# Optimization experiments

Hardware: AMD Instinct MI355X
Metric: run time of the kernel (lower is better)

The kernel has to match this reference:

```python
import jax, jax.numpy as jnp
import numpy as np

N = 128000      # total nodes
B = 128         # graphs, 1000 nodes each
L = 4           # max_levels
S_MAX = 1000    # max cluster size (<= PositionalEncoding max_len)
H = 128         # hidden dim (all conv output dims equal)
IN_DIM = 128
OUT_DIM = 1
E = 1024000
TEMP = 0.1


def layer_norm(x, g, b, eps=1e-5):
    mu = jnp.mean(x, axis=-1, keepdims=True)
    v = jnp.mean((x - mu) ** 2, axis=-1, keepdims=True)
    return (x - mu) * jax.lax.rsqrt(v + eps) * g + b


def transformer_conv(x, src, dst, Wq, bq, Wk, bk, Wv, bv, Ws, bs):
    # PyG TransformerConv, heads=1: softmax over in-edges of each dst node
    q = x @ Wq + bq
    k = x @ Wk + bk
    v = x @ Wv + bv
    logits = jnp.sum(q[dst] * k[src], axis=-1) / jnp.sqrt(jnp.float32(q.shape[-1]))
    m = jax.ops.segment_max(logits, dst, num_segments=N)
    e = jnp.exp(logits - m[dst])
    s = jax.ops.segment_sum(e, dst, num_segments=N)
    alpha = e / s[dst]
    agg = jax.ops.segment_sum(alpha[:, None] * v[src], dst, num_segments=N)
    return agg + x @ Ws + bs  # root_weight skip connection


def pos_encoding(S, d):
    pos = jnp.arange(S, dtype=jnp.float32)[:, None]
    div = jnp.exp(jnp.arange(0, d, 2, dtype=jnp.float32) * (-jnp.log(10000.0) / d))
    pe = jnp.zeros((S, d), jnp.float32)
    pe = pe.at[:, 0::2].set(jnp.sin(pos * div))
    pe = pe.at[:, 1::2].set(jnp.cos(pos * div))
    return pe


def gru(xseq, Wih, Whh, bih, bhh):
    # xseq: [G, S, H] -> outputs [G, S, H]; torch GRU gate math
    G = xseq.shape[0]
    def step(h, x_t):
        gi = x_t @ Wih.T + bih
        gh = h @ Whh.T + bhh
        ir, iz, inn = jnp.split(gi, 3, axis=-1)
        hr, hz, hn = jnp.split(gh, 3, axis=-1)
        r = jax.nn.sigmoid(ir + hr)
        z = jax.nn.sigmoid(iz + hz)
        n = jnp.tanh(inn + r * hn)
        h_new = (1.0 - z) * n + z * h
        return h_new, h_new
    h0 = jnp.zeros((G, Whh.shape[1]), xseq.dtype)
    _, outs = jax.lax.scan(step, h0, jnp.swapaxes(xseq, 0, 1))
    return jnp.swapaxes(outs, 0, 1)


def _forward(x, tree_edge_index, call_sequences, batch,
             conv_Wq, conv_bq, conv_Wk, conv_bk, conv_Wv, conv_bv, conv_Ws, conv_bs,
             ln_g, ln_b, centers, proj_W, proj_b,
             gru_Wih, gru_Whh, gru_bih, gru_bhh, seqln_g, seqln_b,
             lin1_W, lin1_b, lin2_W, lin2_b):
    src, dst = tree_edge_index[0], tree_edge_index[1]
    h = x
    for i in range(3):  # conv1/bn1, conv2/bn2, conv4/bn4
        h = transformer_conv(h, src, dst, conv_Wq[i], conv_bq[i], conv_Wk[i],
                             conv_bk[i], conv_Wv[i], conv_bv[i], conv_Ws[i], conv_bs[i])
        h = jax.nn.relu(layer_norm(h, ln_g[i], ln_b[i]))

    # HierarchicalClassifier: cosine-sim soft assignment + center variance loss
    xn = h / jnp.maximum(jnp.linalg.norm(h, axis=-1, keepdims=True), 1e-8)
    cn = centers / jnp.maximum(jnp.linalg.norm(centers, axis=-1, keepdims=True), 1e-8)
    assign = jax.nn.softmax((xn @ cn.T) / TEMP, axis=-1)
    level_ids = jnp.argmax(assign, axis=1).astype(jnp.int32)
    iu0, iu1 = np.triu_indices(L, k=1)
    dvec = jnp.linalg.norm(centers[iu0] - centers[iu1], axis=-1)
    distance = -jnp.var(dvec, ddof=1)  # torch.var is unbiased

    # ragged gather + pad: group nodes by (graph, cluster), sort by call order
    G = B * L
    group = batch * L + level_ids                       # [N]
    order = jnp.argsort(group * N + call_sequences)     # sort by group, then call
    g_sorted = group[order]
    counts = jax.ops.segment_sum(jnp.ones((N,), jnp.int32), group, num_segments=G)
    starts = jnp.cumsum(counts) - counts
    pos = jnp.arange(N, dtype=jnp.int32) - starts[g_sorted]
    seq = jnp.zeros((G, S_MAX, H), h.dtype).at[g_sorted, pos].set(h[order])

    # SequentialRNN: proj -> pos-enc -> GRU -> LayerNorm -> ReLU (mask unused)
    sin = seq @ proj_W + proj_b + pos_encoding(S_MAX, H)[None]
    outs = gru(sin, gru_Wih, gru_Whh, gru_bih, gru_bhh)
    outs = jax.nn.relu(layer_norm(outs, seqln_g, seqln_b))

    # scatter valid positions back; singleton clusters keep raw features
    node_out = jnp.zeros_like(h).at[order].set(outs[g_sorted, pos])
    singleton = (counts[group] == 1)
    gout = jnp.where(singleton[:, None], h, node_out)

    y = jax.nn.gelu(gout @ lin1_W + lin1_b, approximate=False)
    y = jax.nn.sigmoid(y @ lin2_W + lin2_b)
    return y, distance


def setup_inputs():
    key = jax.random.key(0)
    ks = jax.random.split(key, 16)
    p = lambda k, s: jax.random.normal(k, s, jnp.float32) * 0.02
    return {
        "x": jax.random.normal(ks[0], (N, IN_DIM), jnp.float32),
        "tree_edge_index": jax.random.randint(ks[1], (2, E), 0, N, dtype=jnp.int32),
        "call_sequences": jax.random.permutation(ks[2], N).astype(jnp.int32),
        "batch": (jnp.arange(N, dtype=jnp.int32) * B) // N,  # 1000 nodes per graph
        "conv_Wq": p(ks[3], (3, H, H)), "conv_bq": jnp.zeros((3, H), jnp.float32),
        "conv_Wk": p(ks[4], (3, H, H)), "conv_bk": jnp.zeros((3, H), jnp.float32),
        "conv_Wv": p(ks[5], (3, H, H)), "conv_bv": jnp.zeros((3, H), jnp.float32),
        "conv_Ws": p(ks[6], (3, H, H)), "conv_bs": jnp.zeros((3, H), jnp.float32),
        "ln_g": jnp.ones((3, H), jnp.float32), "ln_b": jnp.zeros((3, H), jnp.float32),
        "centers": jax.random.normal(ks[7], (L, H), jnp.float32),
        "proj_W": p(ks[8], (H, H)), "proj_b": jnp.zeros((H,), jnp.float32),
        "gru_Wih": p(ks[9], (3 * H, H)), "gru_Whh": p(ks[10], (3 * H, H)),
        "gru_bih": jnp.zeros((3 * H,), jnp.float32), "gru_bhh": jnp.zeros((3 * H,), jnp.float32),
        "seqln_g": jnp.ones((H,), jnp.float32), "seqln_b": jnp.zeros((H,), jnp.float32),
        "lin1_W": p(ks[11], (H, 8)), "lin1_b": jnp.zeros((8,), jnp.float32),
        "lin2_W": p(ks[12], (8, OUT_DIM)), "lin2_b": jnp.zeros((OUT_DIM,), jnp.float32),
    }


def reference(x, tree_edge_index, call_sequences, batch,
              conv_Wq, conv_bq, conv_Wk, conv_bk, conv_Wv, conv_bv, conv_Ws, conv_bs,
              ln_g, ln_b, centers, proj_W, proj_b,
              gru_Wih, gru_Whh, gru_bih, gru_bhh, seqln_g, seqln_b,
              lin1_W, lin1_b, lin2_W, lin2_b):
    return _forward(x, tree_edge_index, call_sequences, batch,
                    conv_Wq, conv_bq, conv_Wk, conv_bk, conv_Wv, conv_bv, conv_Ws, conv_bs,
                    ln_g, ln_b, centers, proj_W, proj_b,
                    gru_Wih, gru_Whh, gru_bih, gru_bhh, seqln_g, seqln_b,
                    lin1_W, lin1_b, lin2_W, lin2_b)
```

## Files before the change

### kernel.cpp

```cpp
#include <hip/hip_runtime.h>

#define NN 128000
#define EE 1024000
#define HH 128
#define GG 512
#define SMAX 1000
#define NCHUNK 500

typedef unsigned int u32;
typedef unsigned short u16;

constexpr size_t NH     = (size_t)NN*HH;
constexpr size_t F_H    = 0;
constexpr size_t F_A    = NH;
constexpr size_t F_B    = 2*NH;
constexpr size_t F_NODE = F_A + (size_t)NN*192;
constexpr size_t F_CN   = 3*NH;
constexpr size_t F_WKT  = F_CN   + 512;
constexpr size_t F_WQK  = F_WKT  + 3*16384;
constexpr size_t F_BQK  = F_WQK  + 3*16384;
constexpr size_t F_CW   = F_BQK  + 3*128;
constexpr size_t F_PEW  = F_CW   + 128*384;
constexpr size_t F_PEB  = F_PEW  + 1000*384;
constexpr size_t F_END  = F_PEB  + 1000*128;

constexpr size_t I_ROWP = 0;
constexpr size_t I_CUR  = I_ROWP + NN + 8;
constexpr size_t I_COL  = I_CUR  + NN;
constexpr size_t I_GRP  = I_COL  + EE;
constexpr size_t I_INV  = I_GRP  + NN;
constexpr size_t I_POS  = I_INV  + NN;
constexpr size_t I_GN   = I_POS  + NN;
constexpr size_t I_CNT  = I_GN   + (size_t)GG*SMAX;
constexpr size_t I_CH   = I_CNT  + GG;
constexpr size_t I_BS   = I_CH   + (size_t)NCHUNK*GG;
constexpr size_t I_WT   = I_BS   + 512;
constexpr size_t I_END  = I_WT   + 64*384;

constexpr size_t WS_NEEDED = F_END*4 + I_END*4;

__device__ inline float wredf(float v){
  #pragma unroll
  for (int o = 32; o; o >>= 1) v += __shfl_xor(v, o);
  return v;
}
__device__ inline u32 bf16rne(float f){
  u32 u = __float_as_uint(f);
  return (u + 0x7fffu + ((u >> 16) & 1u)) >> 16;
}
__device__ inline float bf2f(u16 u){
  return __uint_as_float(((u32)u) << 16);
}
__device__ inline float frcp(float x){
#if __has_builtin(__builtin_amdgcn_rcpf)
  return __builtin_amdgcn_rcpf(x);
#else
  return 1.f / x;
#endif
}

typedef _Float16 h2_t __attribute__((ext_vector_type(2)));
__device__ inline float dot2f(u32 w, u32 h, float acc){
#if __has_builtin(__builtin_amdgcn_fdot2)
  return __builtin_amdgcn_fdot2(__builtin_bit_cast(h2_t, w),
                                __builtin_bit_cast(h2_t, h), acc, false);
#else
  float r;
  asm("v_dot2_f32_f16 %0, %1, %2, %3" : "=v"(r) : "v"(w), "v"(h), "v"(acc));
  return r;
#endif
}
#define PIN4(v) asm volatile("" : "+v"((v).x), "+v"((v).y), "+v"((v).z), "+v"((v).w))

__global__ void k_sentinel(float* __restrict__ out, int n, float val){
  int i = blockIdx.x * 256 + threadIdx.x;
  if (i < n) out[i] = val;
}

__global__ void k_zero(int* __restrict__ p){
  p[blockIdx.x * 256 + threadIdx.x] = 0;
}
__global__ void k_hist(const int* __restrict__ dst, int* __restrict__ deg){
  int e = blockIdx.x * 256 + threadIdx.x;
  atomicAdd(&deg[dst[e]], 1);
}
__global__ void k_s1(const int* __restrict__ deg, int* __restrict__ bsum){
  __shared__ int red[256];
  int t = threadIdx.x;
  red[t] = deg[blockIdx.x * 256 + t];
  __syncthreads();
  for (int s = 128; s; s >>= 1){ if (t < s) red[t] += red[t + s]; __syncthreads(); }
  if (!t) bsum[blockIdx.x] = red[0];
}
__global__ void k_s2(int* __restrict__ bsum){
  __shared__ int arr[512];
  int t = threadIdx.x;
  int v0 = (t < NCHUNK) ? bsum[t] : 0;
  arr[t] = v0; __syncthreads();
  for (int off = 1; off < 512; off <<= 1){
    int v = (t >= off) ? arr[t - off] : 0;
    __syncthreads();
    arr[t] += v;
    __syncthreads();
  }
  if (t < NCHUNK) bsum[t] = arr[t] - v0;
}
__global__ void k_s3(const int* __restrict__ bsum, int* __restrict__ row_ptr,
                     int* __restrict__ cursor){
  __shared__ int arr[256];
  int t = threadIdx.x;
  int i = blockIdx.x * 256 + t;
  int v0 = cursor[i];
  arr[t] = v0; __syncthreads();
  for (int off = 1; off < 256; off <<= 1){
    int v = (t >= off) ? arr[t - off] : 0;
    __syncthreads();
    arr[t] += v;
    __syncthreads();
  }
  int exc = arr[t] - v0 + bsum[blockIdx.x];
  row_ptr[i] = exc;
  cursor[i]  = exc;
  if (i == 0) row_ptr[NN] = EE;
}
__global__ void k_scatter(const int* __restrict__ src, const int* __restrict__ dst,
                          int* __restrict__ cursor, int* __restrict__ col){
  int e = blockIdx.x * 256 + threadIdx.x;
  int idx = atomicAdd(&cursor[dst[e]], 1);
  col[idx] = src[e];
}

__global__ void k_setup(const float* __restrict__ centers, float* __restrict__ cn,
                        float* __restrict__ dist_out){
  __shared__ float red[128];
  int t = threadIdx.x;
  for (int l = 0; l < 4; ++l){
    float v = centers[l*128 + t];
    red[t] = v * v; __syncthreads();
    for (int s = 64; s; s >>= 1){ if (t < s) red[t] += red[t + s]; __syncthreads(); }
    float nrm = sqrtf(red[0]);
    __syncthreads();
    cn[l*128 + t] = v / fmaxf(nrm, 1e-8f);
  }
  const int iu0[6] = {0,0,0,1,1,2}, iu1[6] = {1,2,3,2,3,3};
  __shared__ float dv[6];
  for (int p = 0; p < 6; ++p){
    float d = centers[iu0[p]*128 + t] - centers[iu1[p]*128 + t];
    red[t] = d * d; __syncthreads();
    for (int s = 64; s; s >>= 1){ if (t < s) red[t] += red[t + s]; __syncthreads(); }
    if (!t) dv[p] = sqrtf(red[0]);
    __syncthreads();
  }
  if (!t){
    float mean = 0.f;
    for (int p = 0; p < 6; ++p) mean += dv[p];
    mean /= 6.f;
    float var = 0.f;
    for (int p = 0; p < 6; ++p){ float d = dv[p] - mean; var += d * d; }
    var /= 5.f;
    dist_out[0] = -var;
  }
}

__global__ void k_pe(const float* __restrict__ projb, float* __restrict__ peb){
  int p = blockIdx.x, t = threadIdx.x;
  float ex  = (float)(t >> 1) * (-2.0f * 9.210340371976184f / 128.0f);
  float ang = (float)p * expf(ex);
  float v = (t & 1) ? cosf(ang) : sinf(ang);
  peb[p*128 + t] = v + projb[t];
}
__global__ void k_pew(const float* __restrict__ peb, const float* __restrict__ Wih,
                      const float* __restrict__ bih, float* __restrict__ pew){
  int p = blockIdx.x;
  int j = blockIdx.y * 128 + threadIdx.x;
  const float* pb = peb + p*128;
  const float* wr = Wih + (size_t)j*128;
  float acc = bih[j];
  #pragma unroll 4
  for (int m = 0; m < 128; ++m) acc += pb[m] * wr[m];
  pew[(size_t)p*384 + j] = acc;
}
__global__ void k_combw(const float* __restrict__ projW, const float* __restrict__ Wih,
                        float* __restrict__ cw){
  int kk = blockIdx.x;
  int j  = blockIdx.y * 128 + threadIdx.x;
  const float* pr = projW + (size_t)kk*128;
  const float* wr = Wih + (size_t)j*128;
  float acc = 0.f;
  #pragma unroll 4
  for (int m = 0; m < 128; ++m) acc += pr[m] * wr[m];
  cw[(size_t)kk*384 + j] = acc;
}
__global__ void k_tr(const float* __restrict__ Wk, float* __restrict__ wkt){
  int kk = blockIdx.x, l = blockIdx.y, c = threadIdx.x;
  wkt[(size_t)l*16384 + kk*128 + c] = Wk[(size_t)l*16384 + c*128 + kk];
}
__global__ void k_mv(const float* __restrict__ M, const float* __restrict__ v,
                     float* __restrict__ out){
  int l = blockIdx.x, i = threadIdx.x;
  const float* row = M + (size_t)l*16384 + (size_t)i*128;
  const float* vv = v + l*128;
  float acc = 0.f;
  #pragma unroll 4
  for (int j = 0; j < 128; ++j) acc += row[j] * vv[j];
  out[l*128 + i] = acc;
}
__global__ void k_packwhh16(const float* __restrict__ Whh, u32* __restrict__ wt){
  int kp = blockIdx.x;
  int j  = blockIdx.y * 128 + threadIdx.x;
  _Float16 a = (_Float16)Whh[(size_t)j*128 + 2*kp];
  _Float16 b = (_Float16)Whh[(size_t)j*128 + 2*kp + 1];
  u32 lo = (u32)__builtin_bit_cast(u16, a);
  u32 hi = (u32)__builtin_bit_cast(u16, b);
  wt[(size_t)j*64 + kp] = (hi << 16) | lo;
}

__global__ __launch_bounds__(256, 2) void k_gemm(
    const float* __restrict__ X, const float* __restrict__ W, int ldw,
    const float* __restrict__ X2, const float* __restrict__ W2,
    const float* __restrict__ bias, const float* __restrict__ pew,
    const int* __restrict__ pos, float* __restrict__ out,
    u16* __restrict__ outb, int ldo,
    const float* __restrict__ lng, const float* __restrict__ lnb,
    const float* __restrict__ bvv, const int* __restrict__ rowp){
  __shared__ __align__(16) float Wl[64*132];
  __shared__ __align__(16) float Xl[64*132];
  int tid = threadIdx.x;
  int rb = blockIdx.x * 128;
  int cb = blockIdx.y * 128;
  int rg = tid >> 4;
  int cg = tid & 15;
  int kxor = (cg >> 2) & 3;
  float acc[8][8];
  #pragma unroll
  for (int a = 0; a < 8; ++a)
    #pragma unroll
    for (int b = 0; b < 8; ++b) acc[a][b] = 0.f;
  int nhalf = X2 ? 4 : 2;
  for (int half = 0; half < nhalf; ++half){
    const float* Xs = (half < 2) ? X : X2;
    const float* Ws = (half < 2) ? W : W2;
    int ldws = (half < 2) ? ldw : 128;
    int hk = half & 1;
    __syncthreads();
    #pragma unroll
    for (int it = 0; it < 8; ++it){
      int idx = it*256 + tid;
      int kk = idx >> 5, c4 = idx & 31;
      *(float4*)&Wl[kk*132 + c4*4] =
          *(const float4*)&Ws[(size_t)(hk*64 + kk)*ldws + cb + c4*4];
    }
    #pragma unroll
    for (int it = 0; it < 8; ++it){
      int idx = it*256 + tid;
      int r = idx >> 4, c4 = idx & 15;
      float4 xv = *(const float4*)&Xs[(size_t)(rb + r)*128 + hk*64 + c4*4];
      Xl[(c4*4+0)*132 + r] = xv.x;
      Xl[(c4*4+1)*132 + r] = xv.y;
      Xl[(c4*4+2)*132 + r] = xv.z;
      Xl[(c4*4+3)*132 + r] = xv.w;
    }
    __syncthreads();
    #pragma unroll 2
    for (int kk = 0; kk < 64; ++kk){
      int kx = kk ^ kxor;
      float4 wa = *(const float4*)&Wl[kx*132 + cg*8];
      float4 wb = *(const float4*)&Wl[kx*132 + cg*8 + 4];
      float4 xa = *(const float4*)&Xl[kx*132 + rg*8];
      float4 xb = *(const float4*)&Xl[kx*132 + rg*8 + 4];
      float xs[8] = {xa.x, xa.y, xa.z, xa.w, xb.x, xb.y, xb.z, xb.w};
      float ws[8] = {wa.x, wa.y, wa.z, wa.w, wb.x, wb.y, wb.z, wb.w};
      #pragma unroll
      for (int rr = 0; rr < 8; ++rr)
        #pragma unroll
        for (int j = 0; j < 8; ++j) acc[rr][j] += xs[rr] * ws[j];
    }
  }
  if (lng){
    float gv[8], bl[8], bb[8], vv[8];
    #pragma unroll
    for (int j = 0; j < 8; ++j){
      int c = cg*8 + j;
      gv[j] = lng[c]; bl[j] = lnb[c]; bb[j] = bias[c]; vv[j] = bvv[c];
    }
    #pragma unroll
    for (int rr = 0; rr < 8; ++rr){
      int r = rb + rg*8 + rr;
      bool deg = rowp[r+1] > rowp[r];
      float rs = 0.f, rq = 0.f;
      #pragma unroll
      for (int j = 0; j < 8; ++j){
        float v = acc[rr][j] + bb[j] + (deg ? vv[j] : 0.f);
        acc[rr][j] = v;
        rs += v; rq += v*v;
      }
      #pragma unroll
      for (int o = 8; o; o >>= 1){ rs += __shfl_xor(rs, o); rq += __shfl_xor(rq, o); }
      float mu = rs * 0.0078125f;
      float var = rq * 0.0078125f - mu*mu;
      float rstd = rsqrtf(var + 1e-5f);
      float ov[8];
      #pragma unroll
      for (int j = 0; j < 8; ++j)
        ov[j] = fmaxf((acc[rr][j] - mu)*rstd*gv[j] + bl[j], 0.f);
      float* op = out + (size_t)r*128 + cg*8;
      *(float4*)op       = *(const float4*)&ov[0];
      *(float4*)(op + 4) = *(const float4*)&ov[4];
    }
    return;
  }
  #pragma unroll
  for (int rr = 0; rr < 8; ++rr){
    int r = rb + rg*8 + rr;
    float bv[8];
    if (pos){
      const float* pw = pew + (size_t)pos[r]*384 + cb + cg*8;
      #pragma unroll
      for (int j = 0; j < 8; ++j) bv[j] = pw[j];
    } else if (bias){
      #pragma unroll
      for (int j = 0; j < 8; ++j) bv[j] = bias[cb + cg*8 + j];
    } else {
      #pragma unroll
      for (int j = 0; j < 8; ++j) bv[j] = 0.f;
    }
    if (outb){
      u16 ob[8];
      #pragma unroll
      for (int j = 0; j < 8; ++j) ob[j] = (u16)bf16rne(acc[rr][j] + bv[j]);
      *(uint4*)(outb + (size_t)r*ldo + cb + cg*8) = *(const uint4*)ob;
    } else {
      float ov[8];
      #pragma unroll
      for (int j = 0; j < 8; ++j) ov[j] = acc[rr][j] + bv[j];
      float* op = out + (size_t)r*ldo + cb + cg*8;
      *(float4*)op       = *(const float4*)&ov[0];
      *(float4*)(op + 4) = *(const float4*)&ov[4];
    }
  }
}

__global__ __launch_bounds__(256) void k_edge(
    const float* __restrict__ qt, const float* __restrict__ xsrc,
    const int* __restrict__ row_ptr, const int* __restrict__ col,
    float* __restrict__ xagg){
  int d = blockIdx.x * 8 + (threadIdx.x >> 5);
  int lane = threadIdx.x & 31;
  int e0 = row_ptr[d], e1 = row_ptr[d+1];
  if (e0 == e1){
    *(float4*)&xagg[(size_t)d*128 + lane*4] = make_float4(0.f, 0.f, 0.f, 0.f);
    return;
  }
  const float S = 0.08838834764831845f;
  float4 qv = *(const float4*)&qt[(size_t)d*128 + lane*4];
  float ss0 = 0.f, ss1 = 0.f;
  float4 A0 = make_float4(0.f,0.f,0.f,0.f), A1 = make_float4(0.f,0.f,0.f,0.f);
  int e = e0;
  for (; e + 1 < e1; e += 2){
    float4 x0 = *(const float4*)&xsrc[(size_t)col[e]  *128 + lane*4];
    float4 x1 = *(const float4*)&xsrc[(size_t)col[e+1]*128 + lane*4];
    float p0 = qv.x*x0.x + qv.y*x0.y + qv.z*x0.z + qv.w*x0.w;
    float p1 = qv.x*x1.x + qv.y*x1.y + qv.z*x1.z + qv.w*x1.w;
    #pragma unroll
    for (int o = 16; o; o >>= 1){ p0 += __shfl_xor(p0, o); p1 += __shfl_xor(p1, o); }
    float el0 = __expf(p0 * S);
    float el1 = __expf(p1 * S);
    ss0 += el0; ss1 += el1;
    A0.x += el0*x0.x; A0.y += el0*x0.y; A0.z += el0*x0.z; A0.w += el0*x0.w;
    A1.x += el1*x1.x; A1.y += el1*x1.y; A1.z += el1*x1.z; A1.w += el1*x1.w;
  }
  if (e < e1){
    float4 x0 = *(const float4*)&xsrc[(size_t)col[e]*128 + lane*4];
    float p0 = qv.x*x0.x + qv.y*x0.y + qv.z*x0.z + qv.w*x0.w;
    #pragma unroll
    for (int o = 16; o; o >>= 1) p0 += __shfl_xor(p0, o);
    float el0 = __expf(p0 * S);
    ss0 += el0;
    A0.x += el0*x0.x; A0.y += el0*x0.y; A0.z += el0*x0.z; A0.w += el0*x0.w;
  }
  float inv = 1.f / (ss0 + ss1);
  *(float4*)&xagg[(size_t)d*128 + lane*4] =
      make_float4((A0.x+A1.x)*inv, (A0.y+A1.y)*inv, (A0.z+A1.z)*inv, (A0.w+A1.w)*inv);
}

__global__ __launch_bounds__(256) void k_lnrelu_cls(
    const float* __restrict__ in, const float* __restrict__ g,
    const float* __restrict__ b, const float* __restrict__ bvv,
    const int* __restrict__ rowp, float* __restrict__ outp,
    const float* __restrict__ cn, const int* __restrict__ batch,
    const int* __restrict__ callsq, int* __restrict__ grp, int* __restrict__ inv){
  int node = blockIdx.x * 4 + (threadIdx.x >> 6);
  int lane = threadIdx.x & 63;
  float x0 = in[(size_t)node*128 + 2*lane], x1 = in[(size_t)node*128 + 2*lane + 1];
  if (rowp[node+1] > rowp[node]){
    x0 += bvv[2*lane];
    x1 += bvv[2*lane + 1];
  }
  float s = wredf(x0 + x1);
  float qq = wredf(x0*x0 + x1*x1);
  float mu = s * 0.0078125f;
  float var = qq * 0.0078125f - mu*mu;
  float rstd = rsqrtf(var + 1e-5f);
  float y0 = fmaxf((x0 - mu)*rstd*g[2*lane]   + b[2*lane],   0.f);
  float y1 = fmaxf((x1 - mu)*rstd*g[2*lane+1] + b[2*lane+1], 0.f);
  outp[(size_t)node*128 + 2*lane]     = y0;
  outp[(size_t)node*128 + 2*lane + 1] = y1;
  float p0 = y0*cn[      2*lane] + y1*cn[      2*lane+1];
  float p1 = y0*cn[128 + 2*lane] + y1*cn[128 + 2*lane+1];
  float p2 = y0*cn[256 + 2*lane] + y1*cn[256 + 2*lane+1];
  float p3 = y0*cn[384 + 2*lane] + y1*cn[384 + 2*lane+1];
  p0 = wredf(p0); p1 = wredf(p1); p2 = wredf(p2); p3 = wredf(p3);
  if (lane == 0){
    float best = p0; int bi = 0;
    if (p1 > best){ best = p1; bi = 1; }
    if (p2 > best){ best = p2; bi = 2; }
    if (p3 > best){ best = p3; bi = 3; }
    grp[node] = batch[node]*4 + bi;
    inv[callsq[node]] = node;
  }
}

__global__ __launch_bounds__(256) void k_g1(const int* __restrict__ inv,
                                            const int* __restrict__ grp,
                                            int* __restrict__ ch){
  __shared__ int hist[GG];
  int c = blockIdx.x, t = threadIdx.x;
  hist[t] = 0; hist[t + 256] = 0;
  __syncthreads();
  int g = grp[inv[c*256 + t]];
  atomicAdd(&hist[g], 1);
  __syncthreads();
  ch[c*GG + t] = hist[t];
  ch[c*GG + 256 + t] = hist[256 + t];
}
__global__ void k_g2(int* __restrict__ ch, int* __restrict__ cnt){
  __shared__ int arr[512];
  int g = blockIdx.x, t = threadIdx.x;
  int v0 = (t < NCHUNK) ? ch[(size_t)t*GG + g] : 0;
  arr[t] = v0; __syncthreads();
  for (int off = 1; off < 512; off <<= 1){
    int v = (t >= off) ? arr[t - off] : 0;
    __syncthreads();
    arr[t] += v;
    __syncthreads();
  }
  if (t < NCHUNK) ch[(size_t)t*GG + g] = arr[t] - v0;
  if (t == 511) cnt[g] = arr[511];
}
__global__ __launch_bounds__(256) void k_g3(
    const int* __restrict__ inv, const int* __restrict__ grp,
    const int* __restrict__ ch, int* __restrict__ pos, int* __restrict__ gn){
  __shared__ int hist[GG];
  int c = blockIdx.x, t = threadIdx.x;
  hist[t] = 0; hist[t + 256] = 0;
  __syncthreads();
  int node = inv[c*256 + t];
  int g = grp[node];
  int lane = t & 63, w = t >> 6;
  int before = 0, total = 0;
  for (int j = 0; j < 64; ++j){
    int gj = __shfl(g, j);
    if (gj == g){ total++; if (j < lane) before++; }
  }
  int base = 0;
  for (int wv = 0; wv < 4; ++wv){
    if (w == wv){
      base = hist[g];
      if (before == total - 1) hist[g] = base + total;
    }
    __syncthreads();
  }
  int p = ch[c*GG + g] + base + before;
  pos[node] = p;
  gn[(size_t)g*SMAX + p] = node;
}

__global__ __launch_bounds__(256)
__attribute__((amdgpu_waves_per_eu(2, 2)))
void k_gru(
    const u16* __restrict__ gi, const u32* __restrict__ wt,
    const float* __restrict__ bhh, const int* __restrict__ gn,
    const int* __restrict__ cnt, u16* __restrict__ node_out){
  __shared__ __align__(16) u16 hb16[2][128];
  int t = threadIdx.x;
  int j = t >> 1;
  int kh = t & 1;
  int g = blockIdx.x;
  int my = cnt[g];
  if (my <= 1) return;
  uint4 wr_[8], wz_[8], wn_[8];
  {
    const uint4* wt4 = (const uint4*)wt;
    size_t b0 = (size_t)(0*128 + j)*16 + kh*8;
    size_t b1 = (size_t)(1*128 + j)*16 + kh*8;
    size_t b2 = (size_t)(2*128 + j)*16 + kh*8;
    #pragma unroll
    for (int s = 0; s < 8; ++s){
      wr_[s] = wt4[b0 + s];
      wz_[s] = wt4[b1 + s];
      wn_[s] = wt4[b2 + s];
    }
    #pragma unroll
    for (int s = 0; s < 8; ++s){
      PIN4(wr_[s]); PIN4(wz_[s]); PIN4(wn_[s]);
    }
  }
  if (t < 128) hb16[0][t] = 0;
  float br = bhh[j], bz = bhh[128 + j], bn = bhh[256 + j];
  const int* gnr = gn + (size_t)g*SMAX;
  float hprev = 0.f;
  int nA = gnr[0];
  int nB = gnr[min(1, my - 1)];
  int nC = gnr[min(2, my - 1)];
  const u16* gA = gi + (size_t)nA*384;
  const u16* gB = gi + (size_t)nB*384;
  const u16* gC = gi + (size_t)nC*384;
  float axr = bf2f(gA[j]), axz = bf2f(gA[128 + j]), axn = bf2f(gA[256 + j]);
  float bxr = bf2f(gB[j]), bxz = bf2f(gB[128 + j]), bxn = bf2f(gB[256 + j]);
  float cxr = bf2f(gC[j]), cxz = bf2f(gC[128 + j]), cxn = bf2f(gC[256 + j]);
  __syncthreads();
  for (int p = 0; p < my; ++p){
    int cur = p & 1, nxt = cur ^ 1;
    float xr = axr, xz = axz, xn = axn;
    int node = nA;
    axr = bxr; axz = bxz; axn = bxn; nA = nB;
    bxr = cxr; bxz = cxz; bxn = cxn; nB = nC;
    nC = gnr[min(p + 3, my - 1)];
    const u16* gN = gi + (size_t)nC*384;
    cxr = bf2f(gN[j]); cxz = bf2f(gN[128 + j]); cxn = bf2f(gN[256 + j]);
    const uint4* HB = (const uint4*)&hb16[cur][0];
    uint4 hh[8];
    #pragma unroll
    for (int s = 0; s < 8; ++s) hh[s] = HB[kh*8 + s];
    __builtin_amdgcn_s_setprio(1);
    float ar = 0.f, az = 0.f, an = 0.f;
    #pragma unroll
    for (int s = 0; s < 8; ++s){
      ar = dot2f(wr_[s].x, hh[s].x, ar); az = dot2f(wz_[s].x, hh[s].x, az); an = dot2f(wn_[s].x, hh[s].x, an);
      ar = dot2f(wr_[s].y, hh[s].y, ar); az = dot2f(wz_[s].y, hh[s].y, az); an = dot2f(wn_[s].y, hh[s].y, an);
      ar = dot2f(wr_[s].z, hh[s].z, ar); az = dot2f(wz_[s].z, hh[s].z, az); an = dot2f(wn_[s].z, hh[s].z, an);
      ar = dot2f(wr_[s].w, hh[s].w, ar); az = dot2f(wz_[s].w, hh[s].w, az); an = dot2f(wn_[s].w, hh[s].w, an);
    }
    ar += __shfl_xor(ar, 1); az += __shfl_xor(az, 1); an += __shfl_xor(an, 1);
    ar += br; az += bz; an += bn;
    float er = __expf(-(xr + ar));
    float r  = frcp(1.f + er);
    float ez = __expf(-(xz + az));
    float z  = frcp(1.f + ez);
    float y  = xn + r * an;
    float e2 = __expf(-2.f * y);
    float n  = (1.f - e2) * frcp(1.f + e2);
    float hnew = n + z * (hprev - n);
    __builtin_amdgcn_s_setprio(0);
    hprev = hnew;
    if (!kh){
      _Float16 hf = (_Float16)hnew;
      hb16[nxt][j] = __builtin_bit_cast(u16, hf);
      node_out[(size_t)node*128 + j] = (u16)bf16rne(hnew);
    }
    __syncthreads();
  }
}

__global__ __launch_bounds__(256) void k_head(
    const float* __restrict__ h, const u16* __restrict__ node_out,
    const int* __restrict__ grp, const int* __restrict__ cnt,
    const float* __restrict__ sqg, const float* __restrict__ sqb,
    const float* __restrict__ l1W, const float* __restrict__ l1b,
    const float* __restrict__ l2W, const float* __restrict__ l2b,
    float* __restrict__ out){
  int node = blockIdx.x * 4 + (threadIdx.x >> 6);
  int lane = threadIdx.x & 63;
  bool single = (cnt[grp[node]] == 1);
  float x0, x1;
  if (single){
    x0 = h[(size_t)node*128 + 2*lane];
    x1 = h[(size_t)node*128 + 2*lane + 1];
  } else {
    float r0 = bf2f(node_out[(size_t)node*128 + 2*lane]);
    float r1 = bf2f(node_out[(size_t)node*128 + 2*lane + 1]);
    float s = wredf(r0 + r1);
    float qq = wredf(r0*r0 + r1*r1);
    float mu = s * 0.0078125f;
    float var = qq * 0.0078125f - mu*mu;
    float rstd = rsqrtf(var + 1e-5f);
    x0 = fmaxf((r0 - mu)*rstd*sqg[2*lane]   + sqb[2*lane],   0.f);
    x1 = fmaxf((r1 - mu)*rstd*sqg[2*lane+1] + sqb[2*lane+1], 0.f);
  }
  float acc[8];
  #pragma unroll
  for (int j = 0; j < 8; ++j)
    acc[j] = x0 * l1W[(2*lane)*8 + j] + x1 * l1W[(2*lane + 1)*8 + j];
  #pragma unroll
  for (int o = 32; o; o >>= 1)
    #pragma unroll
    for (int j = 0; j < 8; ++j) acc[j] += __shfl_xor(acc[j], o);
  if (lane == 0){
    float zz = l2b[0];
    #pragma unroll
    for (int j = 0; j < 8; ++j){
      float xx = acc[j] + l1b[j];
      float ge = 0.5f * xx * (1.f + erff(xx * 0.7071067811865476f));
      zz += ge * l2W[j];
    }
    out[node] = 1.f / (1.f + expf(-zz));
  }
}

extern "C" void kernel_launch(void* const* d_in, const int* in_sizes, int n_in,
                              void* d_out, int out_size, void* d_ws, size_t ws_size,
                              hipStream_t stream){
  float* out = (float*)d_out;

  if (ws_size < WS_NEEDED){
    float code = -(float)(ws_size >> 20);
    k_sentinel<<<(out_size + 255)/256, 256, 0, stream>>>(out, out_size, code);
    return;
  }

  const float* x       = (const float*)d_in[0];
  const int*   tei     = (const int*)d_in[1];
  const int*   callsq  = (const int*)d_in[2];
  const int*   batch   = (const int*)d_in[3];
  const float* Wq      = (const float*)d_in[4];
  const float* bq      = (const float*)d_in[5];
  const float* Wk      = (const float*)d_in[6];
  const float* bk      = (const float*)d_in[7];
  const float* Wv      = (const float*)d_in[8];
  const float* bv      = (const float*)d_in[9];
  const float* Wsk     = (const float*)d_in[10];
  const float* bsk     = (const float*)d_in[11];
  const float* lng     = (const float*)d_in[12];
  const float* lnb     = (const float*)d_in[13];
  const float* centers = (const float*)d_in[14];
  const float* projW   = (const float*)d_in[15];
  const float* projb   = (const float*)d_in[16];
  const float* Wih     = (const float*)d_in[17];
  const float* Whh     = (const float*)d_in[18];
  const float* bih     = (const float*)d_in[19];
  const float* bhh     = (const float*)d_in[20];
  const float* sqg     = (const float*)d_in[21];
  const float* sqb     = (const float*)d_in[22];
  const float* l1W     = (const float*)d_in[23];
  const float* l1b     = (const float*)d_in[24];
  const float* l2W     = (const float*)d_in[25];
  const float* l2b     = (const float*)d_in[26];

  float* wf = (float*)d_ws;
  float* f_h    = wf + F_H;
  float* f_a    = wf + F_A;
  float* f_b    = wf + F_B;
  float* f_cn   = wf + F_CN;
  float* f_wkt  = wf + F_WKT;
  float* f_wqk  = wf + F_WQK;
  float* f_bqk  = wf + F_BQK;
  float* f_cw   = wf + F_CW;
  float* f_pew  = wf + F_PEW;
  float* f_peb  = wf + F_PEB;
  u16*   gi_bf  = (u16*)(wf + F_A);
  u16*   no_bf  = (u16*)(wf + F_NODE);
  int* wi = (int*)(wf + F_END);
  int* i_rowp = wi + I_ROWP;
  int* i_cur  = wi + I_CUR;
  int* i_col  = wi + I_COL;
  int* i_grp  = wi + I_GRP;
  int* i_inv  = wi + I_INV;
  int* i_pos  = wi + I_POS;
  int* i_gn   = wi + I_GN;
  int* i_cnt  = wi + I_CNT;
  int* i_ch   = wi + I_CH;
  int* i_bs   = wi + I_BS;
  u32* i_wt   = (u32*)(wi + I_WT);

  const int* esrc = tei;
  const int* edst = tei + EE;

  k_zero<<<NN/256, 256, 0, stream>>>(i_cur);
  k_hist<<<EE/256, 256, 0, stream>>>(edst, i_cur);
  k_s1<<<NCHUNK, 256, 0, stream>>>(i_cur, i_bs);
  k_s2<<<1, 512, 0, stream>>>(i_bs);
  k_s3<<<NCHUNK, 256, 0, stream>>>(i_bs, i_rowp, i_cur);
  k_scatter<<<EE/256, 256, 0, stream>>>(esrc, edst, i_cur, i_col);

  k_setup<<<1, 128, 0, stream>>>(centers, f_cn, out + NN);
  k_pe<<<1000, 128, 0, stream>>>(projb, f_peb);
  k_pew<<<dim3(1000, 3), 128, 0, stream>>>(f_peb, Wih, bih, f_pew);
  k_tr<<<dim3(128, 3), 128, 0, stream>>>(Wk, f_wkt);
  for (int i = 0; i < 3; ++i)
    k_gemm<<<dim3(1, 1), 256, 0, stream>>>(Wq + (size_t)i*16384, f_wkt + (size_t)i*16384,
        128, nullptr, nullptr, nullptr, nullptr, nullptr, f_wqk + (size_t)i*16384,
        nullptr, 128, nullptr, nullptr, nullptr, nullptr);
  k_mv<<<3, 128, 0, stream>>>(Wk, bq, f_bqk);
  k_combw<<<dim3(128, 3), 128, 0, stream>>>(projW, Wih, f_cw);
  k_packwhh16<<<dim3(64, 3), 128, 0, stream>>>(Whh, i_wt);

  for (int i = 0; i < 3; ++i){
    const float* xin = i ? f_h : x;
    size_t wo = (size_t)i * 128 * 128, bo = (size_t)i * 128;
    k_gemm<<<dim3(NN/128, 1), 256, 0, stream>>>(xin, f_wqk + (size_t)i*16384, 128,
        nullptr, nullptr, f_bqk + bo, nullptr, nullptr, f_b, nullptr, 128,
        nullptr, nullptr, nullptr, nullptr);
    k_edge<<<NN/8, 256, 0, stream>>>(f_b, xin, i_rowp, i_col, f_a);
    if (i < 2){
      k_gemm<<<dim3(NN/128, 1), 256, 0, stream>>>(f_a, Wv + wo, 128, xin, Wsk + wo,
          bsk + bo, nullptr, nullptr, f_h, nullptr, 128,
          lng + bo, lnb + bo, bv + bo, i_rowp);
    } else {
      k_gemm<<<dim3(NN/128, 1), 256, 0, stream>>>(f_a, Wv + wo, 128, xin, Wsk + wo,
          bsk + bo, nullptr, nullptr, f_b, nullptr, 128,
          nullptr, nullptr, nullptr, nullptr);
      k_lnrelu_cls<<<NN/4, 256, 0, stream>>>(f_b, lng + bo, lnb + bo, bv + bo, i_rowp,
          f_h, f_cn, batch, callsq, i_grp, i_inv);
    }
  }

  k_g1<<<NCHUNK, 256, 0, stream>>>(i_inv, i_grp, i_ch);
  k_g2<<<GG, 512, 0, stream>>>(i_ch, i_cnt);
  k_g3<<<NCHUNK, 256, 0, stream>>>(i_inv, i_grp, i_ch, i_pos, i_gn);

  k_gemm<<<dim3(NN/128, 3), 256, 0, stream>>>(f_h, f_cw, 384, nullptr, nullptr,
      nullptr, f_pew, i_pos, nullptr, gi_bf, 384, nullptr, nullptr, nullptr, nullptr);

  k_gru<<<GG, 256, 0, stream>>>(gi_bf, i_wt, bhh, i_gn, i_cnt, no_bf);

  k_head<<<NN/4, 256, 0, stream>>>(f_h, no_bf, i_grp, i_cnt, sqg, sqb,
                                   l1W, l1b, l2W, l2b, out);
}
```

Before: 2.118 ms.

## Unroll GRU recurrence by four with deeper input prefetch and lighter barriers

Restructures the sequential GRU loop into a 4-step unrolled body that prefetches gate inputs four steps ahead as raw bf16, converting to float only when used. The idea is to hide global load latency behind the recurrent step. It also packs pairs of bf16 outputs via a lane shuffle into 32-bit stores and replaces __syncthreads with an explicit lgkmcnt wait plus s_barrier, skipping the wait on outstanding global stores. The remainder steps run in a scalar tail loop. Costs are extra registers under fixed waves_per_eu and more code size.

```diff
diff --git a/kernel.cpp b/kernel.cpp
--- a/kernel.cpp
+++ b/kernel.cpp
@@ -475,6 +475,46 @@
   gn[(size_t)g*SMAX + p] = node;
 }
 
+#define GRU_STEP(XR, XZ, XN, NODE, CUR, NXT)                                     \
+  {                                                                              \
+    const uint4* HB = (const uint4*)&hb16[CUR][0];                               \
+    uint4 hh[8];                                                                 \
+    _Pragma("unroll")                                                            \
+    for (int s = 0; s < 8; ++s) hh[s] = HB[kh*8 + s];                            \
+    __builtin_amdgcn_s_setprio(1);                                               \
+    float ar = 0.f, az = 0.f, an = 0.f;                                          \
+    _Pragma("unroll")                                                            \
+    for (int s = 0; s < 8; ++s){                                                 \
+      ar = dot2f(wr_[s].x, hh[s].x, ar); az = dot2f(wz_[s].x, hh[s].x, az); an = dot2f(wn_[s].x, hh[s].x, an); \
+      ar = dot2f(wr_[s].y, hh[s].y, ar); az = dot2f(wz_[s].y, hh[s].y, az); an = dot2f(wn_[s].y, hh[s].y, an); \
+      ar = dot2f(wr_[s].z, hh[s].z, ar); az = dot2f(wz_[s].z, hh[s].z, az); an = dot2f(wn_[s].z, hh[s].z, an); \
+      ar = dot2f(wr_[s].w, hh[s].w, ar); az = dot2f(wz_[s].w, hh[s].w, az); an = dot2f(wn_[s].w, hh[s].w, an); \
+    }                                                                            \
+    ar += __shfl_xor(ar, 1); az += __shfl_xor(az, 1); an += __shfl_xor(an, 1);   \
+    ar += br; az += bz; an += bn;                                                \
+    float er = __expf(-((XR) + ar));                                             \
+    float rg_ = frcp(1.f + er);                                                  \
+    float ez = __expf(-((XZ) + az));                                             \
+    float zg_ = frcp(1.f + ez);                                                  \
+    float yv = (XN) + rg_ * an;                                                  \
+    float e2 = __expf(-2.f * yv);                                                \
+    float ng_ = (1.f - e2) * frcp(1.f + e2);                                     \
+    float hnew = ng_ + zg_ * (hprev - ng_);                                      \
+    __builtin_amdgcn_s_setprio(0);                                               \
+    hprev = hnew;                                                                \
+    u16 hbf = (u16)bf16rne(hnew);                                                \
+    u32 pk = ((u32)(u16)__shfl_xor((int)hbf, 2) << 16) | (u32)hbf;               \
+    if (!kh){                                                                    \
+      _Float16 hf16 = (_Float16)hnew;                                            \
+      hb16[NXT][j] = __builtin_bit_cast(u16, hf16);                              \
+    }                                                                            \
+    if ((t & 3) == 0)                                                            \
+      *(u32*)(node_out + (size_t)(NODE)*128 + j) = pk;                           \
+    asm volatile("s_waitcnt lgkmcnt(0)" ::: "memory");                           \
+    __builtin_amdgcn_s_barrier();                                                \
+    asm volatile("" ::: "memory");                                               \
+  }
+
 __global__ __launch_bounds__(256)
 __attribute__((amdgpu_waves_per_eu(2, 2)))
 void k_gru(
@@ -509,56 +549,63 @@
   float br = bhh[j], bz = bhh[128 + j], bn = bhh[256 + j];
   const int* gnr = gn + (size_t)g*SMAX;
   float hprev = 0.f;
-  int nA = gnr[0];
-  int nB = gnr[min(1, my - 1)];
-  int nC = gnr[min(2, my - 1)];
-  const u16* gA = gi + (size_t)nA*384;
-  const u16* gB = gi + (size_t)nB*384;
-  const u16* gC = gi + (size_t)nC*384;
-  float axr = bf2f(gA[j]), axz = bf2f(gA[128 + j]), axn = bf2f(gA[256 + j]);
-  float bxr = bf2f(gB[j]), bxz = bf2f(gB[128 + j]), bxn = bf2f(gB[256 + j]);
-  float cxr = bf2f(gC[j]), cxz = bf2f(gC[128 + j]), cxn = bf2f(gC[256 + j]);
+  int n0 = gnr[0];
+  int n1 = gnr[min(1, my - 1)];
+  int n2 = gnr[min(2, my - 1)];
+  int n3 = gnr[min(3, my - 1)];
+  u16 a0r, a0z, a0n, a1r, a1z, a1n;
+  u16 b0r, b0z, b0n, b1r, b1z, b1n;
+  {
+    const u16* g0 = gi + (size_t)n0*384;
+    const u16* g1 = gi + (size_t)n1*384;
+    a0r = g0[j]; a0z = g0[128 + j]; a0n = g0[256 + j];
+    a1r = g1[j]; a1z = g1[128 + j]; a1n = g1[256 + j];
+    const u16* g2 = gi + (size_t)n2*384;
+    const u16* g3 = gi + (size_t)n3*384;
+    b0r = g2[j]; b0z = g2[128 + j]; b0n = g2[256 + j];
+    b1r = g3[j]; b1z = g3[128 + j]; b1n = g3[256 + j];
+  }
+  int nn0 = gnr[min(4, my - 1)];
+  int nn1 = gnr[min(5, my - 1)];
+  int nn2 = gnr[min(6, my - 1)];
+  int nn3 = gnr[min(7, my - 1)];
   __syncthreads();
-  for (int p = 0; p < my; ++p){
+  int K = my >> 2;
+  for (int k = 0; k < K; ++k){
+    int base = k*4;
+    int n4 = nn0, n5 = nn1, n6 = nn2, n7 = nn3;
+    float x0r = bf2f(a0r), x0z = bf2f(a0z), x0n = bf2f(a0n);
+    float x1r = bf2f(a1r), x1z = bf2f(a1z), x1n = bf2f(a1n);
+    {
+      const u16* g4 = gi + (size_t)n4*384;
+      const u16* g5 = gi + (size_t)n5*384;
+      a0r = g4[j]; a0z = g4[128 + j]; a0n = g4[256 + j];
+      a1r = g5[j]; a1z = g5[128 + j]; a1n = g5[256 + j];
+    }
+    GRU_STEP(x0r, x0z, x0n, n0, 0, 1);
+    GRU_STEP(x1r, x1z, x1n, n1, 1, 0);
+    float x2r = bf2f(b0r), x2z = bf2f(b0z), x2n = bf2f(b0n);
+    float x3r = bf2f(b1r), x3z = bf2f(b1z), x3n = bf2f(b1n);
+    {
+      const u16* g6 = gi + (size_t)n6*384;
+      const u16* g7 = gi + (size_t)n7*384;
+      b0r = g6[j]; b0z = g6[128 + j]; b0n = g6[256 + j];
+      b1r = g7[j]; b1z = g7[128 + j]; b1n = g7[256 + j];
+    }
+    GRU_STEP(x2r, x2z, x2n, n2, 0, 1);
+    GRU_STEP(x3r, x3z, x3n, n3, 1, 0);
+    nn0 = gnr[min(base + 8,  my - 1)];
+    nn1 = gnr[min(base + 9,  my - 1)];
+    nn2 = gnr[min(base + 10, my - 1)];
+    nn3 = gnr[min(base + 11, my - 1)];
+    n0 = n4; n1 = n5; n2 = n6; n3 = n7;
+  }
+  for (int p = K*4; p < my; ++p){
+    int node = gnr[p];
+    const u16* gr = gi + (size_t)node*384;
+    float xr = bf2f(gr[j]), xz = bf2f(gr[128 + j]), xn = bf2f(gr[256 + j]);
     int cur = p & 1, nxt = cur ^ 1;
-    float xr = axr, xz = axz, xn = axn;
-    int node = nA;
-    axr = bxr; axz = bxz; axn = bxn; nA = nB;
-    bxr = cxr; bxz = cxz; bxn = cxn; nB = nC;
-    nC = gnr[min(p + 3, my - 1)];
-    const u16* gN = gi + (size_t)nC*384;
-    cxr = bf2f(gN[j]); cxz = bf2f(gN[128 + j]); cxn = bf2f(gN[256 + j]);
-    const uint4* HB = (const uint4*)&hb16[cur][0];
-    uint4 hh[8];
-    #pragma unroll
-    for (int s = 0; s < 8; ++s) hh[s] = HB[kh*8 + s];
-    __builtin_amdgcn_s_setprio(1);
-    float ar = 0.f, az = 0.f, an = 0.f;
-    #pragma unroll
-    for (int s = 0; s < 8; ++s){
-      ar = dot2f(wr_[s].x, hh[s].x, ar); az = dot2f(wz_[s].x, hh[s].x, az); an = dot2f(wn_[s].x, hh[s].x, an);
-      ar = dot2f(wr_[s].y, hh[s].y, ar); az = dot2f(wz_[s].y, hh[s].y, az); an = dot2f(wn_[s].y, hh[s].y, an);
-      ar = dot2f(wr_[s].z, hh[s].z, ar); az = dot2f(wz_[s].z, hh[s].z, az); an = dot2f(wn_[s].z, hh[s].z, an);
-      ar = dot2f(wr_[s].w, hh[s].w, ar); az = dot2f(wz_[s].w, hh[s].w, az); an = dot2f(wn_[s].w, hh[s].w, an);
-    }
-    ar += __shfl_xor(ar, 1); az += __shfl_xor(az, 1); an += __shfl_xor(an, 1);
-    ar += br; az += bz; an += bn;
-    float er = __expf(-(xr + ar));
-    float r  = frcp(1.f + er);
-    float ez = __expf(-(xz + az));
-    float z  = frcp(1.f + ez);
-    float y  = xn + r * an;
-    float e2 = __expf(-2.f * y);
-    float n  = (1.f - e2) * frcp(1.f + e2);
-    float hnew = n + z * (hprev - n);
-    __builtin_amdgcn_s_setprio(0);
-    hprev = hnew;
-    if (!kh){
-      _Float16 hf = (_Float16)hnew;
-      hb16[nxt][j] = __builtin_bit_cast(u16, hf);
-      node_out[(size_t)node*128 + j] = (u16)bf16rne(hnew);
-    }
-    __syncthreads();
+    GRU_STEP(xr, xz, xn, node, cur, nxt);
   }
 }
 
```

Result: no change. 2.091 ms (-1.3%).
